# Performance work log

Hardware: AMD Instinct MI355X
Metric: run time of the kernel (lower is better)

## Reference

```python
import jax, jax.numpy as jnp
import numpy as np

H = 64
VOCAB = 64
LN_EPS = 1e-5
NORM_EPS = 1e-12


def setup_inputs() -> dict:
    key = jax.random.key(0)
    ks = jax.random.split(key, 16)
    B, L = 256, 2048
    s = 1.0 / np.sqrt(H)
    inp = {
        "seq": jax.random.randint(ks[0], (B, L), 0, VOCAB, dtype=jnp.int32),
        "embed": jax.random.normal(ks[1], (VOCAB, H), jnp.float32),
        "w1": jax.random.normal(ks[2], (H, 2 * H), jnp.float32) * s,
        "b1": jnp.zeros((2 * H,), jnp.float32),
        "w2": jax.random.normal(ks[3], (2 * H, H), jnp.float32) * (1.0 / np.sqrt(2 * H)),
        "b2": jnp.zeros((H,), jnp.float32),
        "ln_g": jnp.ones((H,), jnp.float32),
        "ln_b": jnp.zeros((H,), jnp.float32),
        "wk": jax.random.normal(ks[4], (H, H), jnp.float32) * s,
        "wv": jax.random.normal(ks[5], (H, H), jnp.float32) * s,
        "wq": jax.random.normal(ks[6], (H, H), jnp.float32) * s,
        "wrp": jax.random.normal(ks[7], (H, H), jnp.float32) * s,
        "brp": jnp.zeros((H,), jnp.float32),
        "wout": jax.random.normal(ks[8], (H, VOCAB), jnp.float32) * s,
        "bout": jnp.zeros((VOCAB,), jnp.float32),
    }
    return inp


def _layernorm(x, g, b):
    mu = jnp.mean(x, axis=-1, keepdims=True)
    var = jnp.mean((x - mu) ** 2, axis=-1, keepdims=True)
    return (x - mu) * jax.lax.rsqrt(var + LN_EPS) * g + b


def _forward(seq, embed, w1, b1, w2, b2, ln_g, ln_b, wk, wv, wq, wrp, brp, wout, bout):
    e = embed[seq]                                   # [B, L, H]
    ff = jax.nn.relu(e @ w1 + b1) @ w2 + b2          # [B, L, H]
    hs = _layernorm(e + ff, ln_g, ln_b)              # [B, L, H]
    B, L, _ = hs.shape

    hpre = hs[:, :-1, :]                             # timesteps 0..L-2
    k = hpre @ wk                                    # [B, L-1, H]
    v = hpre @ wv                                    # [B, L-1, H]
    knorm = jnp.linalg.norm(k, axis=-1, keepdims=True)
    kn = k / jnp.maximum(knorm, NORM_EPS)            # F.normalize

    # delta-rule recurrence: M += (v - M k_n) k_n^T, scanned over time
    def step(M, kv):
        k_t, v_t = kv                                # [B, H] each
        vp = jnp.einsum("bij,bj->bi", M, k_t)
        M = M + jnp.einsum("bi,bj->bij", v_t - vp, k_t)
        return M, None

    M0 = jnp.zeros((B, H, H), hs.dtype)
    M, _ = jax.lax.scan(step, M0, (jnp.swapaxes(kn, 0, 1), jnp.swapaxes(v, 0, 1)))

    q = hs[:, -1, :] @ wq                            # [B, H]
    r = jnp.einsum("bij,bj->bi", M, q)               # [B, H]
    return (r @ wrp + brp) @ wout + bout             # [B, VOCAB]


def reference(seq, embed, w1, b1, w2, b2, ln_g, ln_b, wk, wv, wq, wrp, brp, wout, bout):
    return _forward(seq, embed, w1, b1, w2, b2, ln_g, ln_b, wk, wv, wq, wrp, brp, wout, bout)
```

## Files before the change

kernel.cpp:

```cpp
#include <hip/hip_runtime.h>
#include <hip/hip_bf16.h>

#define HH   64
#define H2   128
#define VOC  64
#define LSEQ 2048

__global__ __launch_bounds__(128) void build_tables(
    const float* __restrict__ embed, const float* __restrict__ w1, const float* __restrict__ b1,
    const float* __restrict__ w2, const float* __restrict__ b2,
    const float* __restrict__ ln_g, const float* __restrict__ ln_b,
    const float* __restrict__ wk, const float* __restrict__ wv, const float* __restrict__ wq,
    float* __restrict__ kn_t, float* __restrict__ v_t, float* __restrict__ q_t)
{
    const int tok = blockIdx.x;
    const int tid = threadIdx.x;
    __shared__ float e_lds[HH];
    __shared__ float h_lds[H2];
    __shared__ float hs_lds[HH];

    if (tid < HH) e_lds[tid] = embed[tok * HH + tid];
    __syncthreads();

    {
        float s = b1[tid];
        #pragma unroll 8
        for (int i = 0; i < HH; ++i) s = fmaf(e_lds[i], w1[i * H2 + tid], s);
        h_lds[tid] = fmaxf(s, 0.f);
    }
    __syncthreads();

    if (tid < HH) {
        float f = b2[tid];
        #pragma unroll 8
        for (int j = 0; j < H2; ++j) f = fmaf(h_lds[j], w2[j * HH + tid], f);
        float x = e_lds[tid] + f;
        float sum = x, sq = x * x;
        #pragma unroll
        for (int m = 1; m < 64; m <<= 1) { sum += __shfl_xor(sum, m); sq += __shfl_xor(sq, m); }
        float mu  = sum * (1.f / HH);
        float var = sq * (1.f / HH) - mu * mu;
        hs_lds[tid] = (x - mu) * rsqrtf(var + 1e-5f) * ln_g[tid] + ln_b[tid];
    }
    __syncthreads();

    if (tid < HH) {
        float k = 0.f, v = 0.f, q = 0.f;
        #pragma unroll 8
        for (int j = 0; j < HH; ++j) {
            float h = hs_lds[j];
            k = fmaf(h, wk[j * HH + tid], k);
            v = fmaf(h, wv[j * HH + tid], v);
            q = fmaf(h, wq[j * HH + tid], q);
        }
        float kk = k * k;
        #pragma unroll
        for (int m = 1; m < 64; m <<= 1) kk += __shfl_xor(kk, m);
        float kn = k / fmaxf(sqrtf(kk), 1e-12f);
        kn_t[tok * HH + tid] = kn;
        v_t [tok * HH + tid] = v;
        q_t [tok * HH + tid] = q;
    }
}

__global__ __launch_bounds__(64) void build_dots(
    const float* __restrict__ kn_t, const float* __restrict__ q_t,
    float* __restrict__ w_t, float* __restrict__ cq_t)
{
    const int aa = blockIdx.x, b = threadIdx.x;
    const bool isW = (aa < VOC);
    const int a = isW ? aa : aa - VOC;
    const float* xrow = isW ? (kn_t + a * HH) : (q_t + a * HH);
    __shared__ float xa[HH];
    xa[b] = xrow[b];
    __syncthreads();
    const float4* kav = (const float4*)xa;
    const float4* kbv = (const float4*)(kn_t + b * HH);
    float4 s = {0.f, 0.f, 0.f, 0.f};
    #pragma unroll
    for (int j = 0; j < 16; ++j) {
        float4 x = kav[j], y = kbv[j];
        s.x = fmaf(x.x, y.x, s.x); s.y = fmaf(x.y, y.y, s.y);
        s.z = fmaf(x.z, y.z, s.z); s.w = fmaf(x.w, y.w, s.w);
    }
    float r = (s.x + s.y) + (s.z + s.w);
    (isW ? w_t : cq_t)[a * VOC + b] = r;
}

__global__ __launch_bounds__(64) void build_head(
    const float* __restrict__ v_t, const float* __restrict__ wrp, const float* __restrict__ brp,
    const float* __restrict__ wout, const float* __restrict__ bout,
    float* __restrict__ vpw_t, float* __restrict__ bo_t)
{
    const int b = blockIdx.x, o = threadIdx.x;
    __shared__ float vrow[HH], vp[HH];
    vrow[o] = v_t[b * HH + o];
    __syncthreads();
    float s = 0.f;
    #pragma unroll 8
    for (int i = 0; i < HH; ++i) s = fmaf(vrow[i], wrp[i * HH + o], s);
    vp[o] = s;
    __syncthreads();
    float s2 = 0.f;
    #pragma unroll 8
    for (int i = 0; i < HH; ++i) s2 = fmaf(vp[i], wout[i * VOC + o], s2);
    vpw_t[b * VOC + o] = s2;
    if (b == 0) {
        float t = bout[o];
        #pragma unroll 8
        for (int i = 0; i < HH; ++i) t = fmaf(brp[i], wout[i * VOC + o], t);
        bo_t[o] = t;
    }
}

__device__ __forceinline__ float bf64(float x) {
    int q;
    q = __builtin_amdgcn_mov_dpp(__builtin_bit_cast(int, x), 0xB1,  0xF, 0xF, true); x += __builtin_bit_cast(float, q);
    q = __builtin_amdgcn_mov_dpp(__builtin_bit_cast(int, x), 0x4E,  0xF, 0xF, true); x += __builtin_bit_cast(float, q);
    q = __builtin_amdgcn_mov_dpp(__builtin_bit_cast(int, x), 0x141, 0xF, 0xF, true); x += __builtin_bit_cast(float, q);
    q = __builtin_amdgcn_mov_dpp(__builtin_bit_cast(int, x), 0x140, 0xF, 0xF, true); x += __builtin_bit_cast(float, q);
    q = __builtin_amdgcn_ds_swizzle(__builtin_bit_cast(int, x), 0x401F);             x += __builtin_bit_cast(float, q);
    x += __shfl_xor(x, 32);
    return x;
}

#define PROC(G, ST, SP, SNT, SC, SN, PT, PW, TAIL)                           \
{                                                                            \
    if (PT) {                                                                \
        const int nb_ = 2046 - 8 * ((G) + 2);                                \
        _Pragma("unroll")                                                    \
        for (int j = 0; j < 8; ++j) {                                        \
            int tt = nb_ - j;                                                \
            a[SP][j] = seq_lds[tt < 0 ? 0 : tt];                             \
        }                                                                    \
    }                                                                        \
    if (PW) {                                                                \
        _Pragma("unroll")                                                    \
        for (int j = 0; j < 8; ++j) {                                        \
            wr[SN][j]  = w_lds[(a[SNT][j] << 6) + lane];                     \
            cqv[SN][j] = cq_lds[a[SNT][j]];                                  \
        }                                                                    \
    }                                                                        \
    float d_[8];                                                             \
    _Pragma("unroll")                                                        \
    for (int j = 0; j < 8; ++j) d_[j] = wr[SC][j] * S;                       \
    _Pragma("unroll")                                                        \
    for (int j = 0; j < 8; ++j) d_[j] = bf64(d_[j]);                         \
    int sa_[8];                                                              \
    _Pragma("unroll")                                                        \
    for (int j = 0; j < 8; ++j)                                              \
        sa_[j] = __builtin_amdgcn_readfirstlane(a[ST][j]);                   \
    float gm_[8];                                                            \
    _Pragma("unroll")                                                        \
    for (int j = 0; j < 8; ++j) {                                            \
        float g0_ = cqv[SC][j] - d_[j];                                      \
        _Pragma("unroll")                                                    \
        for (int j2 = 0; j2 < j; ++j2) {                                     \
            float G_ = __builtin_bit_cast(float,                             \
                __builtin_amdgcn_readlane(                                   \
                    __builtin_bit_cast(int, wr[SC][j]), sa_[j2]));           \
            g0_ = fmaf(-G_, gm_[j2], g0_);                                   \
        }                                                                    \
        gm_[j] = g0_;                                                        \
        if (!(TAIL) || j < 7)                                                \
            S += (lane == a[ST][j]) ? g0_ : 0.f;                             \
    }                                                                        \
}

__global__ __launch_bounds__(64) void delta_s_scan(
    const int* __restrict__ seq,
    const float* __restrict__ w_t, const float* __restrict__ cq_t,
    const float* __restrict__ vpw_t, const float* __restrict__ bo_t,
    float* __restrict__ out)
{
    __shared__ __align__(16) float w_lds[VOC * VOC];
    __shared__ __align__(16) int   seq_lds[LSEQ];
    __shared__ float cq_lds[VOC];
    __shared__ float s_lds[VOC];

    const int b    = blockIdx.x;
    const int lane = threadIdx.x;
    const int* __restrict__ seq_b = seq + (long)b * LSEQ;

    {
        const float4* s1 = (const float4*)w_t; float4* d1 = (float4*)w_lds;
        #pragma unroll
        for (int r = 0; r < 16; ++r) d1[lane + 64 * r] = s1[lane + 64 * r];
        const int4* s3 = (const int4*)seq_b; int4* d3 = (int4*)seq_lds;
        #pragma unroll
        for (int r = 0; r < 8; ++r) d3[lane + 64 * r] = s3[lane + 64 * r];
    }
    __syncthreads();
    {
        const int qtok = seq_lds[LSEQ - 1];
        cq_lds[lane] = cq_t[qtok * VOC + lane];
    }
    __syncthreads();

    float S = 0.f;
    int   a[3][8];
    float wr[2][8], cqv[2][8];

    #pragma unroll
    for (int j = 0; j < 8; ++j) a[0][j] = seq_lds[2046 - j];
    #pragma unroll
    for (int j = 0; j < 8; ++j) a[1][j] = seq_lds[2038 - j];
    #pragma unroll
    for (int j = 0; j < 8; ++j) {
        wr[0][j]  = w_lds[(a[0][j] << 6) + lane];
        cqv[0][j] = cq_lds[a[0][j]];
    }

    for (int it = 0; it < 42; ++it) {
        const int g = 6 * it;
        PROC(g + 0, 0, 2, 1, 0, 1, 1, 1, 0)
        PROC(g + 1, 1, 0, 2, 1, 0, 1, 1, 0)
        PROC(g + 2, 2, 1, 0, 0, 1, 1, 1, 0)
        PROC(g + 3, 0, 2, 1, 1, 0, 1, 1, 0)
        PROC(g + 4, 1, 0, 2, 0, 1, 1, 1, 0)
        PROC(g + 5, 2, 1, 0, 1, 0, 1, 1, 0)
    }
    PROC(252, 0, 2, 1, 0, 1, 1, 1, 0)
    PROC(253, 1, 0, 2, 1, 0, 1, 1, 0)
    PROC(254, 2, 1, 0, 0, 1, 0, 1, 0)
    PROC(255, 0, 2, 1, 1, 0, 0, 0, 1)

    s_lds[lane] = S;
    __syncthreads();
    float acc = bo_t[lane];
    #pragma unroll 8
    for (int bb = 0; bb < VOC; ++bb)
        acc = fmaf(s_lds[bb], vpw_t[bb * VOC + lane], acc);
    out[(long)b * VOC + lane] = acc;
}

extern "C" void kernel_launch(void* const* d_in, const int* in_sizes, int n_in,
                              void* d_out, int out_size, void* d_ws, size_t ws_size,
                              hipStream_t stream)
{
    const int*   seq   = (const int*)  d_in[0];
    const float* embed = (const float*)d_in[1];
    const float* w1    = (const float*)d_in[2];
    const float* b1    = (const float*)d_in[3];
    const float* w2    = (const float*)d_in[4];
    const float* b2    = (const float*)d_in[5];
    const float* ln_g  = (const float*)d_in[6];
    const float* ln_b  = (const float*)d_in[7];
    const float* wk    = (const float*)d_in[8];
    const float* wv    = (const float*)d_in[9];
    const float* wq    = (const float*)d_in[10];
    const float* wrp   = (const float*)d_in[11];
    const float* brp   = (const float*)d_in[12];
    const float* wout  = (const float*)d_in[13];
    const float* bout  = (const float*)d_in[14];
    float* out = (float*)d_out;

    float* kn_t  = (float*)d_ws;
    float* v_t   = kn_t  + VOC * HH;
    float* q_t   = v_t   + VOC * HH;
    float* w_t   = q_t   + VOC * HH;
    float* cq_t  = w_t   + VOC * VOC;
    float* vpw_t = cq_t  + VOC * VOC;
    float* bo_t  = vpw_t + VOC * VOC;

    const int B = in_sizes[0] / LSEQ;

    hipLaunchKernelGGL(build_tables, dim3(VOC), dim3(H2), 0, stream,
                       embed, w1, b1, w2, b2, ln_g, ln_b, wk, wv, wq,
                       kn_t, v_t, q_t);
    hipLaunchKernelGGL(build_dots, dim3(2 * VOC), dim3(VOC), 0, stream,
                       kn_t, q_t, w_t, cq_t);
    hipLaunchKernelGGL(build_head, dim3(VOC), dim3(VOC), 0, stream,
                       v_t, wrp, brp, wout, bout, vpw_t, bo_t);
    hipLaunchKernelGGL(delta_s_scan, dim3(B), dim3(HH), 0, stream,
                       seq, w_t, cq_t, vpw_t, bo_t, out);
}
```

Baseline: 245.8 us.

## Track the W·S product incrementally to remove per-step wave reductions

The scan previously recomputed W·S for each of the 8 tokens in a group with a full 64-lane butterfly reduction. It now keeps a per-lane running vector DS = W·S, updated with one FMA per token, and reads the needed entries with readlane. Tokens are stored reversed in LDS and loaded as int4 into scalar registers, which drops the per-lane seq gathers and the cq LDS table. This trades many DPP/shuffle reductions for cheap FMAs and scalar reads, but assumes W is symmetric (dot products of kn) and changes the floating-point accumulation order.

Result: faster. 197.6 us (-19.6%).

```diff
diff --git a/kernel.cpp b/kernel.cpp
--- a/kernel.cpp
+++ b/kernel.cpp
@@ -113,69 +113,65 @@
     }
 }
 
-__device__ __forceinline__ float bf64(float x) {
-    int q;
-    q = __builtin_amdgcn_mov_dpp(__builtin_bit_cast(int, x), 0xB1,  0xF, 0xF, true); x += __builtin_bit_cast(float, q);
-    q = __builtin_amdgcn_mov_dpp(__builtin_bit_cast(int, x), 0x4E,  0xF, 0xF, true); x += __builtin_bit_cast(float, q);
-    q = __builtin_amdgcn_mov_dpp(__builtin_bit_cast(int, x), 0x141, 0xF, 0xF, true); x += __builtin_bit_cast(float, q);
-    q = __builtin_amdgcn_mov_dpp(__builtin_bit_cast(int, x), 0x140, 0xF, 0xF, true); x += __builtin_bit_cast(float, q);
-    q = __builtin_amdgcn_ds_swizzle(__builtin_bit_cast(int, x), 0x401F);             x += __builtin_bit_cast(float, q);
-    x += __shfl_xor(x, 32);
-    return x;
+#define RL(x, s)  __builtin_bit_cast(float, __builtin_amdgcn_readlane(__builtin_bit_cast(int, x), (s)))
+
+#define LDTOK(SLOT, G)                                                       \
+{                                                                            \
+    int4 p0_ = seqr4[2 * (G)];                                               \
+    int4 p1_ = seqr4[2 * (G) + 1];                                           \
+    sa[SLOT][0] = __builtin_amdgcn_readfirstlane(p0_.x);                     \
+    sa[SLOT][1] = __builtin_amdgcn_readfirstlane(p0_.y);                     \
+    sa[SLOT][2] = __builtin_amdgcn_readfirstlane(p0_.z);                     \
+    sa[SLOT][3] = __builtin_amdgcn_readfirstlane(p0_.w);                     \
+    sa[SLOT][4] = __builtin_amdgcn_readfirstlane(p1_.x);                     \
+    sa[SLOT][5] = __builtin_amdgcn_readfirstlane(p1_.y);                     \
+    sa[SLOT][6] = __builtin_amdgcn_readfirstlane(p1_.z);                     \
+    sa[SLOT][7] = __builtin_amdgcn_readfirstlane(p1_.w);                     \
+}
+
+#define LDW(WS, TS)                                                          \
+{                                                                            \
+    _Pragma("unroll")                                                        \
+    for (int j = 0; j < 8; ++j)                                              \
+        wr[WS][j] = w_lds[(sa[TS][j] << 6) + lane];                          \
 }
 
 #define PROC(G, ST, SP, SNT, SC, SN, PT, PW, TAIL)                           \
 {                                                                            \
-    if (PT) {                                                                \
-        const int nb_ = 2046 - 8 * ((G) + 2);                                \
-        _Pragma("unroll")                                                    \
-        for (int j = 0; j < 8; ++j) {                                        \
-            int tt = nb_ - j;                                                \
-            a[SP][j] = seq_lds[tt < 0 ? 0 : tt];                             \
-        }                                                                    \
-    }                                                                        \
-    if (PW) {                                                                \
-        _Pragma("unroll")                                                    \
-        for (int j = 0; j < 8; ++j) {                                        \
-            wr[SN][j]  = w_lds[(a[SNT][j] << 6) + lane];                     \
-            cqv[SN][j] = cq_lds[a[SNT][j]];                                  \
-        }                                                                    \
-    }                                                                        \
-    float d_[8];                                                             \
-    _Pragma("unroll")                                                        \
-    for (int j = 0; j < 8; ++j) d_[j] = wr[SC][j] * S;                       \
-    _Pragma("unroll")                                                        \
-    for (int j = 0; j < 8; ++j) d_[j] = bf64(d_[j]);                         \
-    int sa_[8];                                                              \
-    _Pragma("unroll")                                                        \
-    for (int j = 0; j < 8; ++j)                                              \
-        sa_[j] = __builtin_amdgcn_readfirstlane(a[ST][j]);                   \
+    if (PT) LDTOK(SP, (G) + 2)                                               \
+    if (PW) LDW(SN, SNT)                                                     \
+    float din_[8], cqv_[8];                                                  \
+    _Pragma("unroll")                                                        \
+    for (int j = 0; j < 8; ++j) din_[j] = RL(DS, sa[ST][j]);                 \
+    _Pragma("unroll")                                                        \
+    for (int j = 0; j < 8; ++j) cqv_[j] = RL(CQ, sa[ST][j]);                 \
     float gm_[8];                                                            \
+    float tS_ = 0.f;                                                         \
     _Pragma("unroll")                                                        \
     for (int j = 0; j < 8; ++j) {                                            \
-        float g0_ = cqv[SC][j] - d_[j];                                      \
+        float g0_ = cqv_[j] - din_[j];                                       \
         _Pragma("unroll")                                                    \
         for (int j2 = 0; j2 < j; ++j2) {                                     \
-            float G_ = __builtin_bit_cast(float,                             \
-                __builtin_amdgcn_readlane(                                   \
-                    __builtin_bit_cast(int, wr[SC][j]), sa_[j2]));           \
+            float G_ = RL(wr[SC][j], sa[ST][j2]);                            \
             g0_ = fmaf(-G_, gm_[j2], g0_);                                   \
         }                                                                    \
         gm_[j] = g0_;                                                        \
-        if (!(TAIL) || j < 7)                                                \
-            S += (lane == a[ST][j]) ? g0_ : 0.f;                             \
+        if (!(TAIL) || j < 7) {                                              \
+            DS = fmaf(g0_, wr[SC][j], DS);                                   \
+            tS_ += (lane == sa[ST][j]) ? g0_ : 0.f;                          \
+        }                                                                    \
     }                                                                        \
-}
-
-__global__ __launch_bounds__(64) void delta_s_scan(
+    S += tS_;                                                                \
+}
+
+__global__ __launch_bounds__(64) void delta_ds_scan(
     const int* __restrict__ seq,
     const float* __restrict__ w_t, const float* __restrict__ cq_t,
     const float* __restrict__ vpw_t, const float* __restrict__ bo_t,
     float* __restrict__ out)
 {
     __shared__ __align__(16) float w_lds[VOC * VOC];
-    __shared__ __align__(16) int   seq_lds[LSEQ];
-    __shared__ float cq_lds[VOC];
+    __shared__ __align__(16) int   seq_rev[LSEQ];
     __shared__ float s_lds[VOC];
 
     const int b    = blockIdx.x;
@@ -186,30 +182,26 @@
         const float4* s1 = (const float4*)w_t; float4* d1 = (float4*)w_lds;
         #pragma unroll
         for (int r = 0; r < 16; ++r) d1[lane + 64 * r] = s1[lane + 64 * r];
-        const int4* s3 = (const int4*)seq_b; int4* d3 = (int4*)seq_lds;
-        #pragma unroll
-        for (int r = 0; r < 8; ++r) d3[lane + 64 * r] = s3[lane + 64 * r];
-    }
-    __syncthreads();
-    {
-        const int qtok = seq_lds[LSEQ - 1];
-        cq_lds[lane] = cq_t[qtok * VOC + lane];
-    }
-    __syncthreads();
-
-    float S = 0.f;
-    int   a[3][8];
-    float wr[2][8], cqv[2][8];
-
-    #pragma unroll
-    for (int j = 0; j < 8; ++j) a[0][j] = seq_lds[2046 - j];
-    #pragma unroll
-    for (int j = 0; j < 8; ++j) a[1][j] = seq_lds[2038 - j];
-    #pragma unroll
-    for (int j = 0; j < 8; ++j) {
-        wr[0][j]  = w_lds[(a[0][j] << 6) + lane];
-        cqv[0][j] = cq_lds[a[0][j]];
-    }
+        #pragma unroll 4
+        for (int r = 0; r < 32; ++r) {
+            int m = r * 64 + lane;
+            int idx = 2046 - m;
+            seq_rev[m] = seq_b[idx < 0 ? 0 : idx];
+        }
+    }
+    __syncthreads();
+
+    float CQ;
+    { const int qtok = seq_b[LSEQ - 1]; CQ = cq_t[qtok * VOC + lane]; }
+
+    float DS = 0.f, S = 0.f;
+    int   sa[3][8];
+    float wr[2][8];
+    const int4* seqr4 = (const int4*)seq_rev;
+
+    LDTOK(0, 0)
+    LDTOK(1, 1)
+    LDW(0, 0)
 
     for (int it = 0; it < 42; ++it) {
         const int g = 6 * it;
@@ -272,6 +264,6 @@
                        kn_t, q_t, w_t, cq_t);
     hipLaunchKernelGGL(build_head, dim3(VOC), dim3(VOC), 0, stream,
                        v_t, wrp, brp, wout, bout, vpw_t, bo_t);
-    hipLaunchKernelGGL(delta_s_scan, dim3(B), dim3(HH), 0, stream,
+    hipLaunchKernelGGL(delta_ds_scan, dim3(B), dim3(HH), 0, stream,
                        seq, w_t, cq_t, vpw_t, bo_t, out);
 }
```
